# Kernel optimization log

Hardware: AMD Instinct MI355X
Metric: run time of the kernel (lower is better)

## Reference

```python
import jax, jax.numpy as jnp
import numpy as np

N, M, K, P = 200000, 50000, 32, 15
IN_DIM, OUT_DIM = 128, 256
HID = OUT_DIM // 4
KP_EXTENT = 0.05
KP_RADIUS = 0.06
EPS = 1e-5
SLOPE = 0.1


def _lrelu(x):
    return jnp.where(x > 0, x, SLOPE * x)


def _conv1d_bn_lrelu(x, W, b, g, beta):
    # pointwise conv (1x1) + batch-norm over points + leaky relu
    x = x @ W + b
    mu = jnp.mean(x, axis=0)
    var = jnp.var(x, axis=0)
    x = (x - mu) * jax.lax.rsqrt(var + EPS) * g + beta
    return _lrelu(x)


def _kpconv_pool(points, sub_points, pools, feats, kernel_points, kp_w):
    # KPConv with strided pooling: query = sub_points [M,3], support = points [N,3]
    nbr_pts = points[pools] - sub_points[:, None, :]              # [M,K,3] relative neighbor coords
    diff = nbr_pts[:, :, None, :] - kernel_points[None, None]     # [M,K,P,3]
    dist = jnp.sqrt(jnp.sum(diff * diff, axis=-1))                # [M,K,P]
    w = jnp.maximum(0.0, 1.0 - dist / KP_EXTENT)                  # linear correlation influence
    nbr_f = feats[pools]                                          # [M,K,C]
    agg = jnp.einsum('mkp,mkc->mpc', w, nbr_f)                    # per-kernel-point aggregation
    return jnp.einsum('mpc,pcd->md', agg, kp_w)                   # [M,C_out]


def setup_inputs() -> dict:
    key = jax.random.key(0)
    ks = jax.random.split(key, 10)
    points = jax.random.uniform(ks[0], (N, 3), dtype=jnp.float32) * 0.1
    sub_points = jax.random.uniform(ks[1], (M, 3), dtype=jnp.float32) * 0.1
    features = jax.random.normal(ks[2], (N, IN_DIM), dtype=jnp.float32)
    pools = jax.random.randint(ks[3], (M, K), 0, N, dtype=jnp.int32)
    kernel_points = jax.random.uniform(ks[4], (P, 3), minval=-KP_RADIUS, maxval=KP_RADIUS, dtype=jnp.float32)
    s_in = 1.0 / np.sqrt(IN_DIM)
    s_h = 1.0 / np.sqrt(HID)
    W1 = jax.random.normal(ks[5], (IN_DIM, HID), dtype=jnp.float32) * s_in
    kp_w = jax.random.normal(ks[6], (P, HID, HID), dtype=jnp.float32) * s_h
    W2 = jax.random.normal(ks[7], (HID, OUT_DIM), dtype=jnp.float32) * s_h
    Ws = jax.random.normal(ks[8], (IN_DIM, OUT_DIM), dtype=jnp.float32) * s_in
    return dict(
        points=points, sub_points=sub_points, features=features, pools=pools,
        kernel_points=kernel_points,
        W1=W1, b1=jnp.zeros((HID,)), g1=jnp.ones((HID,)), be1=jnp.zeros((HID,)),
        kp_w=kp_w,
        W2=W2, b2=jnp.zeros((OUT_DIM,)), g2=jnp.ones((OUT_DIM,)), be2=jnp.zeros((OUT_DIM,)),
        Ws=Ws, bs=jnp.zeros((OUT_DIM,)), gs=jnp.ones((OUT_DIM,)), bes=jnp.zeros((OUT_DIM,)),
    )


def reference(points, sub_points, features, pools, kernel_points,
              W1, b1, g1, be1, kp_w, W2, b2, g2, be2, Ws, bs, gs, bes):
    # main branch: Conv1D -> KPConvPools -> leaky_relu -> Conv1D
    x = _conv1d_bn_lrelu(features, W1, b1, g1, be1)               # [N,HID]
    x = _kpconv_pool(points, sub_points, pools, x, kernel_points, kp_w)  # [M,HID]
    x = _lrelu(x)
    x = _conv1d_bn_lrelu(x, W2, b2, g2, be2)                      # [M,OUT]
    # shortcut: MaxPoolNeighbors -> Conv1D
    sc = jnp.max(features[pools], axis=1)                         # [M,IN]
    sc = _conv1d_bn_lrelu(sc, Ws, bs, gs, bes)                    # [M,OUT]
    return _lrelu(x + sc)
```

## Files before the change

kernel.cpp:

```cpp
#include <hip/hip_runtime.h>

typedef unsigned short ushort_t;
typedef unsigned int uint_t;
typedef __attribute__((ext_vector_type(8))) short bf8_t;
typedef __attribute__((ext_vector_type(4))) float f4_t;
typedef __attribute__((ext_vector_type(4))) unsigned int u4_t;

#define NPTS 200000
#define MSUB 50000
#define KNBR 32
#define PK 15
#define INDIM 128
#define OUTDIM 256
#define HID 64
#define QD2 1024
#define NB1 1563
#define NBT 1563

__device__ __forceinline__ ushort_t f2bf(float f) {
  uint_t u = __float_as_uint(f);
  u = (u + 0x7fffu + ((u >> 16) & 1u)) >> 16;
  return (ushort_t)u;
}
__device__ __forceinline__ float bf2f(ushort_t h) {
  return __uint_as_float(((uint_t)h) << 16);
}
__device__ __forceinline__ float lrelu(float x) { return fmaxf(x, 0.1f * x); }
__device__ __forceinline__ f4_t zero4() { f4_t z = {0.f, 0.f, 0.f, 0.f}; return z; }

__global__ void prep_w_kernel(const float* __restrict__ W1, const float* __restrict__ W2,
                              const float* __restrict__ Ws, const float* __restrict__ kpw,
                              ushort_t* __restrict__ W1t, ushort_t* __restrict__ W2t,
                              ushort_t* __restrict__ Wst, ushort_t* __restrict__ kpwT2) {
  const int base = blockIdx.x * blockDim.x + threadIdx.x;
  const int stride = gridDim.x * blockDim.x;
  for (int t = base; t < HID * INDIM; t += stride) {
    int c = t & 63, k = t >> 6;
    W1t[c * INDIM + k] = f2bf(W1[k * HID + c]);
  }
  for (int t = base; t < OUTDIM * HID; t += stride) {
    int c = t & 255, k = t >> 8;
    W2t[c * HID + k] = f2bf(W2[k * OUTDIM + c]);
  }
  for (int t = base; t < OUTDIM * INDIM; t += stride) {
    int c = t & 255, k = t >> 8;
    Wst[c * INDIM + k] = f2bf(Ws[k * OUTDIM + c]);
  }
  for (int t = base; t < HID * QD2; t += stride) {
    int d = t >> 10, s = t & 1023;
    int nl = s & 1, r16v = (s >> 1) & 15, gv = (s >> 5) & 3, nh = (s >> 7) & 1, rr = (s >> 8) & 3;
    int p = gv * 4 + rr, c = r16v + (nh * 2 + nl) * 16;
    float v = (p < PK) ? kpw[((long)p * HID + c) * HID + d] : 0.f;
    kpwT2[d * QD2 + s] = f2bf(v);
  }
}

__global__ __launch_bounds__(256) void conv1_kernel(const float* __restrict__ feat,
                                                    const ushort_t* __restrict__ W1t,
                                                    ushort_t* __restrict__ feat16,
                                                    ushort_t* __restrict__ x1,
                                                    float* __restrict__ part1) {
  const int tid = threadIdx.x, wid = tid >> 6, lane = tid & 63;
  const int g = lane >> 4, r16 = lane & 15;
  const int rowbase = blockIdx.x * 128 + wid * 32;
  f4_t acc[2][4];
#pragma unroll
  for (int mi = 0; mi < 2; ++mi)
#pragma unroll
    for (int ni = 0; ni < 4; ++ni) acc[mi][ni] = zero4();
#pragma unroll
  for (int kc = 0; kc < 4; ++kc) {
    const int k0 = kc * 32 + g * 8;
    bf8_t a[2], b[4];
#pragma unroll
    for (int mi = 0; mi < 2; ++mi) {
      const int row = rowbase + mi * 16 + r16;
      const int rowc = (row < NPTS) ? row : 0;
      const float4 f0 = *(const float4*)(feat + (long)rowc * INDIM + k0);
      const float4 f1 = *(const float4*)(feat + (long)rowc * INDIM + k0 + 4);
      a[mi][0] = (short)f2bf(f0.x); a[mi][1] = (short)f2bf(f0.y);
      a[mi][2] = (short)f2bf(f0.z); a[mi][3] = (short)f2bf(f0.w);
      a[mi][4] = (short)f2bf(f1.x); a[mi][5] = (short)f2bf(f1.y);
      a[mi][6] = (short)f2bf(f1.z); a[mi][7] = (short)f2bf(f1.w);
      if (row < NPTS) *(bf8_t*)(feat16 + (long)row * INDIM + k0) = a[mi];
    }
#pragma unroll
    for (int ni = 0; ni < 4; ++ni)
      b[ni] = *(const bf8_t*)(W1t + (r16 + ni * 16) * INDIM + k0);
#pragma unroll
    for (int mi = 0; mi < 2; ++mi)
#pragma unroll
      for (int ni = 0; ni < 4; ++ni)
        acc[mi][ni] = __builtin_amdgcn_mfma_f32_16x16x32_bf16(a[mi], b[ni], acc[mi][ni], 0, 0, 0);
  }
  __shared__ float red[2][64];
  if (tid < 64) { red[0][tid] = 0.f; red[1][tid] = 0.f; }
  __syncthreads();
  float cs[4] = {0.f, 0.f, 0.f, 0.f}, cq[4] = {0.f, 0.f, 0.f, 0.f};
#pragma unroll
  for (int mi = 0; mi < 2; ++mi)
#pragma unroll
    for (int rr = 0; rr < 4; ++rr) {
      const int row = rowbase + mi * 16 + g * 4 + rr;
      if (row < NPTS) {
#pragma unroll
        for (int ni = 0; ni < 4; ++ni) {
          const float v = acc[mi][ni][rr];
          cs[ni] += v;
          cq[ni] += v * v;
          x1[(long)row * HID + r16 + ni * 16] = f2bf(v);
        }
      }
    }
#pragma unroll
  for (int ni = 0; ni < 4; ++ni) {
    atomicAdd(&red[0][r16 + ni * 16], cs[ni]);
    atomicAdd(&red[1][r16 + ni * 16], cq[ni]);
  }
  __syncthreads();
  if (tid < 128) {
    const float v = (tid < 64) ? red[0][tid] : red[1][tid - 64];
    part1[(long)tid * NB1 + blockIdx.x] = v;
  }
}

__global__ __launch_bounds__(256) void reduce1fin_kernel(const float* __restrict__ part1,
                                                         const float* __restrict__ g1,
                                                         const float* __restrict__ be1,
                                                         float* __restrict__ st) {
  const int c = blockIdx.x, tid = threadIdx.x;
  const int slot = (tid < 128) ? c : (64 + c);
  const float* src = part1 + (long)slot * NB1;
  float acc = 0.f;
  for (int i = tid & 127; i < NB1; i += 128) acc += src[i];
  __shared__ float sm[256];
  sm[tid] = acc;
  __syncthreads();
  for (int s = 64; s > 0; s >>= 1) {
    if ((tid & 127) < s) sm[tid] += sm[tid + s];
    __syncthreads();
  }
  if (tid == 0) {
    const float mu = sm[0] / (float)NPTS;
    const float var = sm[128] / (float)NPTS - mu * mu;
    const float a = g1[c] * rsqrtf(var + 1e-5f);
    st[c] = a;
    st[64 + c] = be1[c] - mu * a;
  }
}

__global__ __launch_bounds__(512, 4) void gkp_kernel(
    const float* __restrict__ points, const float* __restrict__ subp,
    const int* __restrict__ pools, const float* __restrict__ kp,
    const ushort_t* __restrict__ x1, const ushort_t* __restrict__ feat16,
    const float* __restrict__ st, const ushort_t* __restrict__ kpwT2,
    ushort_t* __restrict__ x2, ushort_t* __restrict__ scmax) {
  const int tid = threadIdx.x, wid = tid >> 6, lane = tid & 63;
  const int g = lane >> 4, r16 = lane & 15, l31 = lane & 31, hi = lane >> 5;
  const int mbase = blockIdx.x * 16;
  __shared__ __align__(16) char aggT[16 * 2048];
  __shared__ __align__(16) uint_t ft2[8][32][36];
  float A4[4], S4[4];
#pragma unroll
  for (int ni = 0; ni < 4; ++ni) {
    A4[ni] = st[r16 + ni * 16];
    S4[ni] = st[64 + r16 + ni * 16];
  }
  const int p = r16;
  const int pc = (p < PK) ? p : 0;
  const float kx = kp[pc * 3 + 0], ky = kp[pc * 3 + 1], kz = kp[pc * 3 + 2];

#pragma unroll
  for (int mm = 0; mm < 2; ++mm) {
    const int lm = wid * 2 + mm;
    const int m = mbase + lm;
    const int idx0 = pools[m * KNBR + l31];
    float px = 0.f, py = 0.f, pz = 0.f;
    if (lane < 32) {
      px = points[idx0 * 3 + 0];
      py = points[idx0 * 3 + 1];
      pz = points[idx0 * 3 + 2];
    }
#pragma unroll
    for (int i = 0; i < 16; ++i) {
      const int k = 2 * i + hi;
      const int n = __shfl(idx0, k);
      ft2[wid][l31][k] = *(const uint_t*)(x1 + (long)n * HID + l31 * 2);
    }
    const float sx = subp[m * 3 + 0], sy = subp[m * 3 + 1], sz = subp[m * 3 + 2];
    const float kxx = kx + sx, kyy = ky + sy, kzz = kz + sz;
    bf8_t afrag;
#pragma unroll
    for (int j = 0; j < 8; ++j) {
      const int k = g * 8 + j;
      const float dx = __shfl(px, k) - kxx;
      const float dy = __shfl(py, k) - kyy;
      const float dz = __shfl(pz, k) - kzz;
      const float dist = sqrtf(dx * dx + dy * dy + dz * dz);
      float w = fmaxf(0.f, 1.f - dist * 20.f);
      if (p >= PK) w = 0.f;
      afrag[j] = (short)f2bf(w);
    }
    f4_t acc[4];
#pragma unroll
    for (int ni = 0; ni < 4; ++ni) acc[ni] = zero4();
#pragma unroll
    for (int ni = 0; ni < 4; ++ni) {
      const int c = r16 + ni * 16;
      const int c2 = c >> 1;
      const int sh = (c & 1) * 16;
      const float A = A4[ni], S = S4[ni];
      const uint_t* src = &ft2[wid][c2][g * 8];
      const u4_t v0 = *(const u4_t*)src;
      const u4_t v1 = *(const u4_t*)(src + 4);
      bf8_t bfrag;
#pragma unroll
      for (int j = 0; j < 4; ++j) {
        const float xa = __uint_as_float(((v0[j] >> sh) & 0xffffu) << 16);
        bfrag[j] = (short)f2bf(lrelu(A * xa + S));
        const float xb = __uint_as_float(((v1[j] >> sh) & 0xffffu) << 16);
        bfrag[4 + j] = (short)f2bf(lrelu(A * xb + S));
      }
      acc[ni] = __builtin_amdgcn_mfma_f32_16x16x32_bf16(afrag, bfrag, acc[ni], 0, 0, 0);
    }
    char* rowp = aggT + lm * 2048;
#pragma unroll
    for (int rr = 0; rr < 4; ++rr)
#pragma unroll
      for (int nh = 0; nh < 2; ++nh) {
        const uint_t v =
            (uint_t)f2bf(acc[nh * 2][rr]) | ((uint_t)f2bf(acc[nh * 2 + 1][rr]) << 16);
        int byte = ((rr * 2 + nh) * 64 + g * 16 + r16) * 4;
        byte ^= (lm & 7) << 4;
        *(uint_t*)(rowp + byte) = v;
      }
    float mx0 = -3.0e38f, mx1 = -3.0e38f;
#pragma unroll
    for (int k = 0; k < KNBR; ++k) {
      const int n = __shfl(idx0, k);
      const uint_t v = *(const uint_t*)(feat16 + (long)n * INDIM + lane * 2);
      mx0 = fmaxf(mx0, __uint_as_float(v << 16));
      mx1 = fmaxf(mx1, __uint_as_float(v & 0xffff0000u));
    }
    ((uint_t*)scmax)[(long)m * 64 + lane] =
        (uint_t)(__float_as_uint(mx0) >> 16) | (__float_as_uint(mx1) & 0xffff0000u);
  }
  __syncthreads();
  if (wid < 4) {
    f4_t acc2 = zero4();
    const ushort_t* brow = kpwT2 + (long)(wid * 16 + r16) * QD2;
#pragma unroll 8
    for (int kc = 0; kc < 32; ++kc) {
      int byte = (kc * 64 + g * 16) ^ ((r16 & 7) << 4);
      const bf8_t a = *(const bf8_t*)(aggT + r16 * 2048 + byte);
      const bf8_t b = *(const bf8_t*)(brow + kc * 32 + g * 8);
      acc2 = __builtin_amdgcn_mfma_f32_16x16x32_bf16(a, b, acc2, 0, 0, 0);
    }
#pragma unroll
    for (int rr = 0; rr < 4; ++rr) {
      const int m = mbase + g * 4 + rr;
      x2[(long)m * HID + wid * 16 + r16] = f2bf(lrelu(acc2[rr]));
    }
  }
}

template <int KD>
__device__ __forceinline__ void convT_body(const ushort_t* __restrict__ A,
                                           const ushort_t* __restrict__ Bt,
                                           ushort_t* __restrict__ Oraw,
                                           float* __restrict__ part, int blk) {
  const int tid = threadIdx.x, lane = tid & 63;
  const int wid = tid >> 6;
  const int g = lane >> 4, r16 = lane & 15;
  const int rowbase = blk * 32;
  const int colbase = wid * 64;
  f4_t acc[2][4];
#pragma unroll
  for (int mi = 0; mi < 2; ++mi)
#pragma unroll
    for (int ni = 0; ni < 4; ++ni) acc[mi][ni] = zero4();
#pragma unroll
  for (int kc = 0; kc < KD / 32; ++kc) {
    const int k0 = kc * 32 + g * 8;
    bf8_t a[2], b[4];
#pragma unroll
    for (int mi = 0; mi < 2; ++mi) {
      int row = rowbase + mi * 16 + r16;
      if (row >= MSUB) row = 0;
      a[mi] = *(const bf8_t*)(A + (long)row * KD + k0);
    }
#pragma unroll
    for (int ni = 0; ni < 4; ++ni)
      b[ni] = *(const bf8_t*)(Bt + (long)(colbase + r16 + ni * 16) * KD + k0);
#pragma unroll
    for (int mi = 0; mi < 2; ++mi)
#pragma unroll
      for (int ni = 0; ni < 4; ++ni)
        acc[mi][ni] = __builtin_amdgcn_mfma_f32_16x16x32_bf16(a[mi], b[ni], acc[mi][ni], 0, 0, 0);
  }
  __shared__ float red[2][256];
  red[0][tid] = 0.f;
  red[1][tid] = 0.f;
  __syncthreads();
  float cs[4] = {0.f, 0.f, 0.f, 0.f}, cq[4] = {0.f, 0.f, 0.f, 0.f};
#pragma unroll
  for (int mi = 0; mi < 2; ++mi)
#pragma unroll
    for (int rr = 0; rr < 4; ++rr) {
      const int row = rowbase + mi * 16 + g * 4 + rr;
      if (row < MSUB) {
#pragma unroll
        for (int ni = 0; ni < 4; ++ni) {
          const float v = acc[mi][ni][rr];
          cs[ni] += v;
          cq[ni] += v * v;
          Oraw[(long)row * OUTDIM + colbase + r16 + ni * 16] = f2bf(v);
        }
      }
    }
#pragma unroll
  for (int ni = 0; ni < 4; ++ni) {
    atomicAdd(&red[0][colbase + r16 + ni * 16], cs[ni]);
    atomicAdd(&red[1][colbase + r16 + ni * 16], cq[ni]);
  }
  __syncthreads();
  part[(long)tid * NBT + blk] = red[0][tid];
  part[(long)(256 + tid) * NBT + blk] = red[1][tid];
}

__global__ __launch_bounds__(256) void convT_merged_kernel(
    const ushort_t* __restrict__ x2, const ushort_t* __restrict__ W2t,
    const ushort_t* __restrict__ scmax, const ushort_t* __restrict__ Wst,
    ushort_t* __restrict__ x3, ushort_t* __restrict__ scraw,
    float* __restrict__ part2, float* __restrict__ part3) {
  const int b = blockIdx.x;
  if (b < NBT)
    convT_body<HID>(x2, W2t, x3, part2, b);
  else
    convT_body<INDIM>(scmax, Wst, scraw, part3, b - NBT);
}

__global__ __launch_bounds__(256) void reduce23fin_kernel(const float* __restrict__ part2,
                                                          const float* __restrict__ part3,
                                                          const float* __restrict__ g2,
                                                          const float* __restrict__ be2,
                                                          const float* __restrict__ gs,
                                                          const float* __restrict__ bes,
                                                          float* __restrict__ st) {
  const int blk = blockIdx.x, tid = threadIdx.x;
  const int sc = blk >> 8, c = blk & 255;
  const float* part = sc ? part3 : part2;
  const int slot = (tid < 128) ? c : (256 + c);
  const float* src = part + (long)slot * NBT;
  float acc = 0.f;
  for (int i = tid & 127; i < NBT; i += 128) acc += src[i];
  __shared__ float sm[256];
  sm[tid] = acc;
  __syncthreads();
  for (int s = 64; s > 0; s >>= 1) {
    if ((tid & 127) < s) sm[tid] += sm[tid + s];
    __syncthreads();
  }
  if (tid == 0) {
    const float mu = sm[0] / (float)MSUB;
    const float var = sm[128] / (float)MSUB - mu * mu;
    const float a = (sc ? gs : g2)[c] * rsqrtf(var + 1e-5f);
    const int off = sc ? 640 : 128;
    st[off + c] = a;
    st[off + 256 + c] = (sc ? bes : be2)[c] - mu * a;
  }
}

__global__ __launch_bounds__(256) void final_kernel(const ushort_t* __restrict__ x3,
                                                    const ushort_t* __restrict__ sc,
                                                    const float* __restrict__ st,
                                                    float* __restrict__ out) {
  const int i = blockIdx.x * 256 + threadIdx.x;
  const int c0 = (i * 4) & 255;
  const uint2 xv = ((const uint2*)x3)[i];
  const uint2 sv = ((const uint2*)sc)[i];
  float xs[4] = {bf2f((ushort_t)(xv.x & 0xffffu)), bf2f((ushort_t)(xv.x >> 16)),
                 bf2f((ushort_t)(xv.y & 0xffffu)), bf2f((ushort_t)(xv.y >> 16))};
  float ss[4] = {bf2f((ushort_t)(sv.x & 0xffffu)), bf2f((ushort_t)(sv.x >> 16)),
                 bf2f((ushort_t)(sv.y & 0xffffu)), bf2f((ushort_t)(sv.y >> 16))};
  float r[4];
#pragma unroll
  for (int j = 0; j < 4; ++j) {
    const int c = c0 + j;
    const float v = lrelu(st[128 + c] * xs[j] + st[384 + c]);
    const float u = lrelu(st[640 + c] * ss[j] + st[896 + c]);
    r[j] = lrelu(v + u);
  }
  ((float4*)out)[i] = make_float4(r[0], r[1], r[2], r[3]);
}

extern "C" void kernel_launch(void* const* d_in, const int* in_sizes, int n_in,
                              void* d_out, int out_size, void* d_ws, size_t ws_size,
                              hipStream_t stream) {
  (void)in_sizes; (void)n_in; (void)out_size;
  const float* points = (const float*)d_in[0];
  const float* subp = (const float*)d_in[1];
  const float* feat = (const float*)d_in[2];
  const int* pools = (const int*)d_in[3];
  const float* kp = (const float*)d_in[4];
  const float* W1 = (const float*)d_in[5];
  const float* g1 = (const float*)d_in[7];
  const float* be1 = (const float*)d_in[8];
  const float* kpw = (const float*)d_in[9];
  const float* W2 = (const float*)d_in[10];
  const float* g2 = (const float*)d_in[12];
  const float* be2 = (const float*)d_in[13];
  const float* Wsm = (const float*)d_in[14];
  const float* gs = (const float*)d_in[16];
  const float* bes = (const float*)d_in[17];
  float* out = (float*)d_out;

  char* w = (char*)d_ws;
  size_t o = 0;
  ushort_t* feat16 = (ushort_t*)(w + o); o += (size_t)NPTS * INDIM * 2;
  ushort_t* x1 = (ushort_t*)(w + o);     o += (size_t)NPTS * HID * 2;
  ushort_t* x2 = (ushort_t*)(w + o);     o += (size_t)MSUB * HID * 2;
  ushort_t* x3 = (ushort_t*)(w + o);     o += (size_t)MSUB * OUTDIM * 2;
  ushort_t* scmax = (ushort_t*)(w + o);  o += (size_t)MSUB * INDIM * 2;
  ushort_t* scraw = (ushort_t*)(w + o);  o += (size_t)MSUB * OUTDIM * 2;
  float* part1 = (float*)(w + o);        o += (size_t)128 * NB1 * 4;
  float* part2 = (float*)(w + o);        o += (size_t)512 * NBT * 4;
  float* part3 = (float*)(w + o);        o += (size_t)512 * NBT * 4;
  ushort_t* W1t = (ushort_t*)(w + o);    o += HID * INDIM * 2;
  ushort_t* W2t = (ushort_t*)(w + o);    o += OUTDIM * HID * 2;
  ushort_t* Wst = (ushort_t*)(w + o);    o += OUTDIM * INDIM * 2;
  ushort_t* kpwT2 = (ushort_t*)(w + o);  o += HID * QD2 * 2;
  float* st = (float*)(w + o);           o += 1152 * 4;
  if (ws_size < o) return;

  prep_w_kernel<<<64, 256, 0, stream>>>(W1, W2, Wsm, kpw, W1t, W2t, Wst, kpwT2);
  conv1_kernel<<<NB1, 256, 0, stream>>>(feat, W1t, feat16, x1, part1);
  reduce1fin_kernel<<<64, 256, 0, stream>>>(part1, g1, be1, st);
  gkp_kernel<<<MSUB / 16, 512, 0, stream>>>(points, subp, pools, kp, x1, feat16, st,
                                            kpwT2, x2, scmax);
  convT_merged_kernel<<<2 * NBT, 256, 0, stream>>>(x2, W2t, scmax, Wst, x3, scraw,
                                                   part2, part3);
  reduce23fin_kernel<<<512, 256, 0, stream>>>(part2, part3, g2, be2, gs, bes, st);
  final_kernel<<<MSUB * OUTDIM / 1024, 256, 0, stream>>>(x3, scraw, st, out);
}
```

Baseline: 272.4 us.

## Fuse W2 and shortcut 1x1 convs into the KPConv gather kernel

Merges the separate conv-transpose kernel into the gather/KPConv kernel. Each 16-row block now keeps the aggregated x2 and the shortcut max-pool result in shared memory and immediately runs the W2 and Ws matmuls there. It writes raw outputs plus per-block BN partial sums, reduced with wave shuffles instead of shared atomics. This removes the global round trip of x2 and scmax and one kernel launch. In exchange it doubles the number of partial-sum slots, since blocks now cover 16 rows instead of 32, adds work and shared memory to an already heavy kernel, and loads the weights redundantly from every block.

```diff
diff --git a/kernel.cpp b/kernel.cpp
--- a/kernel.cpp
+++ b/kernel.cpp
@@ -15,7 +15,7 @@
 #define HID 64
 #define QD2 1024
 #define NB1 1563
-#define NBT 1563
+#define NBG 3125
 
 __device__ __forceinline__ ushort_t f2bf(float f) {
   uint_t u = __float_as_uint(f);
@@ -149,17 +149,22 @@
   }
 }
 
-__global__ __launch_bounds__(512, 4) void gkp_kernel(
+__global__ __launch_bounds__(512, 4) void gkpc_kernel(
     const float* __restrict__ points, const float* __restrict__ subp,
     const int* __restrict__ pools, const float* __restrict__ kp,
     const ushort_t* __restrict__ x1, const ushort_t* __restrict__ feat16,
     const float* __restrict__ st, const ushort_t* __restrict__ kpwT2,
-    ushort_t* __restrict__ x2, ushort_t* __restrict__ scmax) {
+    const ushort_t* __restrict__ W2t, const ushort_t* __restrict__ Wst,
+    ushort_t* __restrict__ x3, ushort_t* __restrict__ scraw,
+    float* __restrict__ part2, float* __restrict__ part3) {
   const int tid = threadIdx.x, wid = tid >> 6, lane = tid & 63;
   const int g = lane >> 4, r16 = lane & 15, l31 = lane & 31, hi = lane >> 5;
-  const int mbase = blockIdx.x * 16;
+  const int blk = blockIdx.x;
+  const int mbase = blk * 16;
   __shared__ __align__(16) char aggT[16 * 2048];
-  __shared__ __align__(16) uint_t ft2[8][32][36];
+  __shared__ __align__(16) char ftraw[8 * 32 * 36 * 4];
+  __shared__ __align__(16) char scmaxT[16 * 256];
+  uint_t (*ft2)[32][36] = (uint_t (*)[32][36])ftraw;
   float A4[4], S4[4];
 #pragma unroll
   for (int ni = 0; ni < 4; ++ni) {
@@ -242,10 +247,15 @@
       mx0 = fmaxf(mx0, __uint_as_float(v << 16));
       mx1 = fmaxf(mx1, __uint_as_float(v & 0xffff0000u));
     }
-    ((uint_t*)scmax)[(long)m * 64 + lane] =
-        (uint_t)(__float_as_uint(mx0) >> 16) | (__float_as_uint(mx1) & 0xffff0000u);
-  }
-  __syncthreads();
+    {
+      const int chunk = (lane >> 2) ^ (lm & 7);
+      const uint_t v =
+          (uint_t)(__float_as_uint(mx0) >> 16) | (__float_as_uint(mx1) & 0xffff0000u);
+      *(uint_t*)(scmaxT + lm * 256 + chunk * 16 + (lane & 3) * 4) = v;
+    }
+  }
+  __syncthreads();
+  char* x2T = ftraw;
   if (wid < 4) {
     f4_t acc2 = zero4();
     const ushort_t* brow = kpwT2 + (long)(wid * 16 + r16) * QD2;
@@ -256,88 +266,96 @@
       const bf8_t b = *(const bf8_t*)(brow + kc * 32 + g * 8);
       acc2 = __builtin_amdgcn_mfma_f32_16x16x32_bf16(a, b, acc2, 0, 0, 0);
     }
+    const int col = wid * 16 + r16;
 #pragma unroll
     for (int rr = 0; rr < 4; ++rr) {
-      const int m = mbase + g * 4 + rr;
-      x2[(long)m * HID + wid * 16 + r16] = f2bf(lrelu(acc2[rr]));
-    }
-  }
-}
-
-template <int KD>
-__device__ __forceinline__ void convT_body(const ushort_t* __restrict__ A,
-                                           const ushort_t* __restrict__ Bt,
-                                           ushort_t* __restrict__ Oraw,
-                                           float* __restrict__ part, int blk) {
-  const int tid = threadIdx.x, lane = tid & 63;
-  const int wid = tid >> 6;
-  const int g = lane >> 4, r16 = lane & 15;
-  const int rowbase = blk * 32;
-  const int colbase = wid * 64;
-  f4_t acc[2][4];
-#pragma unroll
-  for (int mi = 0; mi < 2; ++mi)
-#pragma unroll
-    for (int ni = 0; ni < 4; ++ni) acc[mi][ni] = zero4();
-#pragma unroll
-  for (int kc = 0; kc < KD / 32; ++kc) {
-    const int k0 = kc * 32 + g * 8;
-    bf8_t a[2], b[4];
-#pragma unroll
-    for (int mi = 0; mi < 2; ++mi) {
-      int row = rowbase + mi * 16 + r16;
-      if (row >= MSUB) row = 0;
-      a[mi] = *(const bf8_t*)(A + (long)row * KD + k0);
-    }
-#pragma unroll
-    for (int ni = 0; ni < 4; ++ni)
-      b[ni] = *(const bf8_t*)(Bt + (long)(colbase + r16 + ni * 16) * KD + k0);
-#pragma unroll
-    for (int mi = 0; mi < 2; ++mi)
+      const int row = g * 4 + rr;
+      const int chunk = (col >> 3) ^ (row & 7);
+      *(ushort_t*)(x2T + row * 128 + chunk * 16 + (col & 7) * 2) = f2bf(lrelu(acc2[rr]));
+    }
+  } else {
+    const int w4 = wid - 4;
+    f4_t cS[4];
+#pragma unroll
+    for (int ni = 0; ni < 4; ++ni) cS[ni] = zero4();
+#pragma unroll
+    for (int kc = 0; kc < 4; ++kc) {
+      const int chunk = (kc * 4 + g) ^ (r16 & 7);
+      const bf8_t aS = *(const bf8_t*)(scmaxT + r16 * 256 + chunk * 16);
+      bf8_t bS[4];
 #pragma unroll
       for (int ni = 0; ni < 4; ++ni)
-        acc[mi][ni] = __builtin_amdgcn_mfma_f32_16x16x32_bf16(a[mi], b[ni], acc[mi][ni], 0, 0, 0);
-  }
-  __shared__ float red[2][256];
-  red[0][tid] = 0.f;
-  red[1][tid] = 0.f;
-  __syncthreads();
-  float cs[4] = {0.f, 0.f, 0.f, 0.f}, cq[4] = {0.f, 0.f, 0.f, 0.f};
-#pragma unroll
-  for (int mi = 0; mi < 2; ++mi)
+        bS[ni] = *(const bf8_t*)(Wst + (long)(w4 * 64 + r16 + ni * 16) * INDIM + kc * 32 + g * 8);
+#pragma unroll
+      for (int ni = 0; ni < 4; ++ni)
+        cS[ni] = __builtin_amdgcn_mfma_f32_16x16x32_bf16(aS, bS[ni], cS[ni], 0, 0, 0);
+    }
+    float cs[4] = {0.f, 0.f, 0.f, 0.f}, cq[4] = {0.f, 0.f, 0.f, 0.f};
 #pragma unroll
     for (int rr = 0; rr < 4; ++rr) {
-      const int row = rowbase + mi * 16 + g * 4 + rr;
-      if (row < MSUB) {
-#pragma unroll
-        for (int ni = 0; ni < 4; ++ni) {
-          const float v = acc[mi][ni][rr];
-          cs[ni] += v;
-          cq[ni] += v * v;
-          Oraw[(long)row * OUTDIM + colbase + r16 + ni * 16] = f2bf(v);
-        }
+      const int row = mbase + g * 4 + rr;
+#pragma unroll
+      for (int ni = 0; ni < 4; ++ni) {
+        const float v = cS[ni][rr];
+        cs[ni] += v;
+        cq[ni] += v * v;
+        scraw[(long)row * OUTDIM + w4 * 64 + r16 + ni * 16] = f2bf(v);
       }
     }
 #pragma unroll
-  for (int ni = 0; ni < 4; ++ni) {
-    atomicAdd(&red[0][colbase + r16 + ni * 16], cs[ni]);
-    atomicAdd(&red[1][colbase + r16 + ni * 16], cq[ni]);
-  }
-  __syncthreads();
-  part[(long)tid * NBT + blk] = red[0][tid];
-  part[(long)(256 + tid) * NBT + blk] = red[1][tid];
-}
-
-__global__ __launch_bounds__(256) void convT_merged_kernel(
-    const ushort_t* __restrict__ x2, const ushort_t* __restrict__ W2t,
-    const ushort_t* __restrict__ scmax, const ushort_t* __restrict__ Wst,
-    ushort_t* __restrict__ x3, ushort_t* __restrict__ scraw,
-    float* __restrict__ part2, float* __restrict__ part3) {
-  const int b = blockIdx.x;
-  if (b < NBT)
-    convT_body<HID>(x2, W2t, x3, part2, b);
-  else
-    convT_body<INDIM>(scmax, Wst, scraw, part3, b - NBT);
+    for (int ni = 0; ni < 4; ++ni) {
+      cs[ni] += __shfl_xor(cs[ni], 16); cs[ni] += __shfl_xor(cs[ni], 32);
+      cq[ni] += __shfl_xor(cq[ni], 16); cq[ni] += __shfl_xor(cq[ni], 32);
+    }
+    if (g == 0) {
+#pragma unroll
+      for (int ni = 0; ni < 4; ++ni) {
+        const int col = w4 * 64 + r16 + ni * 16;
+        part3[(long)col * NBG + blk] = cs[ni];
+        part3[(long)(256 + col) * NBG + blk] = cq[ni];
+      }
+    }
+  }
+  __syncthreads();
+  f4_t c2[2];
+  c2[0] = zero4(); c2[1] = zero4();
+#pragma unroll
+  for (int kc = 0; kc < 2; ++kc) {
+    const int chunk = (kc * 4 + g) ^ (r16 & 7);
+    const bf8_t a2 = *(const bf8_t*)(x2T + r16 * 128 + chunk * 16);
+    bf8_t b2[2];
+#pragma unroll
+    for (int ni = 0; ni < 2; ++ni)
+      b2[ni] = *(const bf8_t*)(W2t + (long)(wid * 32 + r16 + ni * 16) * HID + kc * 32 + g * 8);
+#pragma unroll
+    for (int ni = 0; ni < 2; ++ni)
+      c2[ni] = __builtin_amdgcn_mfma_f32_16x16x32_bf16(a2, b2[ni], c2[ni], 0, 0, 0);
+  }
+  float cs2[2] = {0.f, 0.f}, cq2[2] = {0.f, 0.f};
+#pragma unroll
+  for (int rr = 0; rr < 4; ++rr) {
+    const int row = mbase + g * 4 + rr;
+#pragma unroll
+    for (int ni = 0; ni < 2; ++ni) {
+      const float v = c2[ni][rr];
+      cs2[ni] += v;
+      cq2[ni] += v * v;
+      x3[(long)row * OUTDIM + wid * 32 + r16 + ni * 16] = f2bf(v);
+    }
+  }
+#pragma unroll
+  for (int ni = 0; ni < 2; ++ni) {
+    cs2[ni] += __shfl_xor(cs2[ni], 16); cs2[ni] += __shfl_xor(cs2[ni], 32);
+    cq2[ni] += __shfl_xor(cq2[ni], 16); cq2[ni] += __shfl_xor(cq2[ni], 32);
+  }
+  if (g == 0) {
+#pragma unroll
+    for (int ni = 0; ni < 2; ++ni) {
+      const int col = wid * 32 + r16 + ni * 16;
+      part2[(long)col * NBG + blk] = cs2[ni];
+      part2[(long)(256 + col) * NBG + blk] = cq2[ni];
+    }
+  }
 }
 
 __global__ __launch_bounds__(256) void reduce23fin_kernel(const float* __restrict__ part2,
@@ -351,9 +369,9 @@
   const int sc = blk >> 8, c = blk & 255;
   const float* part = sc ? part3 : part2;
   const int slot = (tid < 128) ? c : (256 + c);
-  const float* src = part + (long)slot * NBT;
+  const float* src = part + (long)slot * NBG;
   float acc = 0.f;
-  for (int i = tid & 127; i < NBT; i += 128) acc += src[i];
+  for (int i = tid & 127; i < NBG; i += 128) acc += src[i];
   __shared__ float sm[256];
   sm[tid] = acc;
   __syncthreads();
@@ -419,13 +437,11 @@
   size_t o = 0;
   ushort_t* feat16 = (ushort_t*)(w + o); o += (size_t)NPTS * INDIM * 2;
   ushort_t* x1 = (ushort_t*)(w + o);     o += (size_t)NPTS * HID * 2;
-  ushort_t* x2 = (ushort_t*)(w + o);     o += (size_t)MSUB * HID * 2;
   ushort_t* x3 = (ushort_t*)(w + o);     o += (size_t)MSUB * OUTDIM * 2;
-  ushort_t* scmax = (ushort_t*)(w + o);  o += (size_t)MSUB * INDIM * 2;
   ushort_t* scraw = (ushort_t*)(w + o);  o += (size_t)MSUB * OUTDIM * 2;
   float* part1 = (float*)(w + o);        o += (size_t)128 * NB1 * 4;
-  float* part2 = (float*)(w + o);        o += (size_t)512 * NBT * 4;
-  float* part3 = (float*)(w + o);        o += (size_t)512 * NBT * 4;
+  float* part2 = (float*)(w + o);        o += (size_t)512 * NBG * 4;
+  float* part3 = (float*)(w + o);        o += (size_t)512 * NBG * 4;
   ushort_t* W1t = (ushort_t*)(w + o);    o += HID * INDIM * 2;
   ushort_t* W2t = (ushort_t*)(w + o);    o += OUTDIM * HID * 2;
   ushort_t* Wst = (ushort_t*)(w + o);    o += OUTDIM * INDIM * 2;
@@ -436,10 +452,8 @@
   prep_w_kernel<<<64, 256, 0, stream>>>(W1, W2, Wsm, kpw, W1t, W2t, Wst, kpwT2);
   conv1_kernel<<<NB1, 256, 0, stream>>>(feat, W1t, feat16, x1, part1);
   reduce1fin_kernel<<<64, 256, 0, stream>>>(part1, g1, be1, st);
-  gkp_kernel<<<MSUB / 16, 512, 0, stream>>>(points, subp, pools, kp, x1, feat16, st,
-                                            kpwT2, x2, scmax);
-  convT_merged_kernel<<<2 * NBT, 256, 0, stream>>>(x2, W2t, scmax, Wst, x3, scraw,
-                                                   part2, part3);
+  gkpc_kernel<<<NBG, 512, 0, stream>>>(points, subp, pools, kp, x1, feat16, st, kpwT2,
+                                       W2t, Wst, x3, scraw, part2, part3);
   reduce23fin_kernel<<<512, 256, 0, stream>>>(part2, part3, g2, be2, gs, bes, st);
   final_kernel<<<MSUB * OUTDIM / 1024, 256, 0, stream>>>(x3, scraw, st, out);
 }
```

Measured after the change: 287.5 us. +5.5%, slower.
